# Optimization experiments

Hardware: AMD Instinct MI355X
Metric: run time of the kernel (lower is better)

## Reference

```python
import jax, jax.numpy as jnp
import numpy as np
from jax import lax

EPS = 1e-5

def conv3x3(x, w):
    # x: [B,C,H,W], w: [O,C,3,3]
    return lax.conv_general_dilated(x, w, (1, 1), ((1, 1), (1, 1)),
                                    dimension_numbers=("NCHW", "OIHW", "NCHW"))

def convbnrelu(x, w, bn):
    gamma, beta, mean, var = bn  # each [C]
    y = conv3x3(x, w)
    scale = (gamma / jnp.sqrt(var + EPS))[:, None, None]
    shift = (beta - mean * gamma / jnp.sqrt(var + EPS))[:, None, None]
    return jax.nn.relu(y * scale + shift)

def conv1x1(x, w, b):
    # w: [O,C,1,1], b: [O]
    return jnp.einsum("bchw,oc->bohw", x, w[:, :, 0, 0]) + b[:, None, None]

def pam(x, wb, bb, wc, bc, wd, bd, alpha, lfm=None):
    B, C, H, W = x.shape
    N = H * W
    q = conv1x1(x, wb, bb)
    k = conv1x1(x, wc, bc)
    v = conv1x1(x, wd, bd)
    if lfm is not None:  # VFAM: qkv flags all 1 -> multiply q, k, v
        q = q * lfm
        k = k * lfm
        v = v * lfm
    fb = q.reshape(B, -1, N).transpose(0, 2, 1)           # [B,N,Cq]
    fc = k.reshape(B, -1, N)                              # [B,Cq,N]
    attn = jax.nn.softmax(jnp.matmul(fb, fc), axis=-1)    # [B,N,N]
    fd = v.reshape(B, C, N)                               # [B,C,N]
    fe = jnp.matmul(fd, attn.transpose(0, 2, 1)).reshape(B, C, H, W)
    return alpha * fe + x

def cam(x, beta):
    B, C, H, W = x.shape
    N = H * W
    fa = x.reshape(B, C, N)
    attn = jnp.matmul(fa, fa.transpose(0, 2, 1))          # [B,C,C]
    attn = jnp.max(attn, axis=-1, keepdims=True) - attn
    attn = jax.nn.softmax(attn, axis=-1)
    fe = jnp.matmul(attn, fa).reshape(B, C, H, W)
    return beta * fe + x

def setup_inputs() -> dict:
    key = jax.random.key(0)
    ks = iter(jax.random.split(key, 64))
    B, Cin, H, W = 2, 2048, 64, 64
    Cmid = Cin // 4         # 512
    Cq = Cmid // 8          # 64
    nclass = 19

    def bn_pack(C):
        g = jnp.ones((C,)) + 0.1 * jax.random.normal(next(ks), (C,))
        b = 0.1 * jax.random.normal(next(ks), (C,))
        m = 0.1 * jax.random.normal(next(ks), (C,))
        v = jax.random.uniform(next(ks), (C,), minval=0.5, maxval=1.5)
        return jnp.stack([g, b, m, v])  # [4,C]

    def conv_w(O, I, kk):
        return jax.random.normal(next(ks), (O, I, kk, kk)) * (1.0 / np.sqrt(I * kk * kk))

    inp = {
        "x": jax.random.normal(next(ks), (B, Cin, H, W)),
        "loss_factor_map": jax.random.uniform(next(ks), (H, W)),
        "wp1": conv_w(Cmid, Cin, 3), "bnp1": bn_pack(Cmid),
        "wp2": conv_w(Cmid, Cmid, 3), "bnp2": bn_pack(Cmid),
        "wc1": conv_w(Cmid, Cin, 3), "bnc1": bn_pack(Cmid),
        "wc2": conv_w(Cmid, Cmid, 3), "bnc2": bn_pack(Cmid),
        "wv1": conv_w(Cmid, Cin, 3), "bnv1": bn_pack(Cmid),
        "wv2": conv_w(Cmid, Cmid, 3), "bnv2": bn_pack(Cmid),
        "pam_wb": conv_w(Cq, Cmid, 1), "pam_bb": jnp.zeros((Cq,)),
        "pam_wc": conv_w(Cq, Cmid, 1), "pam_bc": jnp.zeros((Cq,)),
        "pam_wd": conv_w(Cmid, Cmid, 1), "pam_bd": jnp.zeros((Cmid,)),
        "pam_alpha": 0.3 * jnp.ones((1,)),
        "cam_beta": 0.3 * jnp.ones((1,)),
        "vfam_wb": conv_w(Cq, Cmid, 1), "vfam_bb": jnp.zeros((Cq,)),
        "vfam_wc": conv_w(Cq, Cmid, 1), "vfam_bc": jnp.zeros((Cq,)),
        "vfam_wd": conv_w(Cmid, Cmid, 1), "vfam_bd": jnp.zeros((Cmid,)),
        "vfam_alpha": 0.3 * jnp.ones((1,)),
        "out_w": conv_w(nclass, Cmid, 1), "out_b": jnp.zeros((nclass,)),
        "p3_w": conv_w(nclass, Cmid, 1), "p3_b": jnp.zeros((nclass,)),
        "c3_w": conv_w(nclass, Cmid, 1), "c3_b": jnp.zeros((nclass,)),
    }
    return inp

def reference(x, loss_factor_map,
              wp1, bnp1, wp2, bnp2, wc1, bnc1, wc2, bnc2, wv1, bnv1, wv2, bnv2,
              pam_wb, pam_bb, pam_wc, pam_bc, pam_wd, pam_bd, pam_alpha,
              cam_beta,
              vfam_wb, vfam_bb, vfam_wc, vfam_bc, vfam_wd, vfam_bd, vfam_alpha,
              out_w, out_b, p3_w, p3_b, c3_w, c3_b):
    lfm = loss_factor_map[None, None, :, :]  # (1,1,H,W)
    # Position branch
    fp = convbnrelu(x, wp1, bnp1)
    fp = pam(fp, pam_wb, pam_bb, pam_wc, pam_bc, pam_wd, pam_bd, pam_alpha)
    fp = convbnrelu(fp, wp2, bnp2)
    # Channel branch
    fc = convbnrelu(x, wc1, bnc1)
    fc = cam(fc, cam_beta)
    fc = convbnrelu(fc, wc2, bnc2)
    # Visual-field branch (qkv_vfa_flag = [1,1,1])
    fv = convbnrelu(x, wv1, bnv1)
    fv = pam(fv, vfam_wb, vfam_bb, vfam_wc, vfam_bc, vfam_wd, vfam_bd, vfam_alpha, lfm=lfm)
    fv = convbnrelu(fv, wv2, bnv2)
    # Fusion + heads (Dropout in eval mode = identity)
    fusion = fp + fc + fv
    fusion_out = conv1x1(fusion, out_w, out_b)
    p_out = conv1x1(fp, p3_w, p3_b)
    c_out = conv1x1(fc, c3_w, c3_b)
    return (fusion_out, p_out, c_out)
```

## Files before the change

kernel.cpp:

```cpp
#include <hip/hip_runtime.h>

typedef unsigned short u16;
typedef short s16x8 __attribute__((ext_vector_type(8)));
typedef u16 u16x8 __attribute__((ext_vector_type(8)));
typedef u16 u16x4 __attribute__((ext_vector_type(4)));
typedef float f32x4 __attribute__((ext_vector_type(4)));

#define DEV __device__ __forceinline__

DEV float bf2f(u16 x) { unsigned v = ((unsigned)x) << 16; float f; __builtin_memcpy(&f, &v, 4); return f; }
DEV u16 f2bf(float f) { unsigned u; __builtin_memcpy(&u, &f, 4); u += 0x7FFFu + ((u >> 16) & 1u); return (u16)(u >> 16); }

DEV void gload16(const u16* g, u16* l) {
  __builtin_amdgcn_global_load_lds((const __attribute__((address_space(1))) void*)g,
                                   (__attribute__((address_space(3))) void*)l, 16, 0, 0);
}

__global__ void detect_dtype(const u16* __restrict__ x, int* __restrict__ flag) {
  int tid = threadIdx.x;
  float mx = 0.f;
  for (int i = tid; i < 4096; i += 256) mx = fmaxf(mx, fabsf(bf2f(x[i])));
  __shared__ float red[4];
  int wave = tid >> 6, lane = tid & 63;
  for (int off = 32; off; off >>= 1) mx = fmaxf(mx, __shfl_xor(mx, off));
  if (lane == 0) red[wave] = mx;
  __syncthreads();
  if (tid == 0) {
    mx = fmaxf(fmaxf(red[0], red[1]), fmaxf(red[2], red[3]));
    *flag = (mx > 1e4f) ? 1 : 0;
  }
}

struct CvBatch {
  const void* src[28];
  unsigned dstOff[28];
  unsigned n[28];
  unsigned chunkStart[29];
  int cnt;
};

__global__ __launch_bounds__(256) void convert_batch(CvBatch cb, u16* __restrict__ dstBase,
                                                     const int* __restrict__ flag) {
  const int isF = *flag;
  const unsigned bid = blockIdx.x;
  int j = 0;
  while (bid >= cb.chunkStart[j + 1]) ++j;
  const unsigned base = (bid - cb.chunkStart[j]) * 2048 + threadIdx.x * 8;
  const unsigned n = cb.n[j];
  if (base >= n) return;
  u16* dst = dstBase + cb.dstOff[j];
  const void* src = cb.src[j];
  if (base + 8 <= n) {
    u16x8 v;
    if (isF) {
      const float* f = (const float*)src;
#pragma unroll
      for (int k = 0; k < 8; ++k) v[k] = f2bf(f[base + k]);
    } else {
      v = *(const u16x8*)&((const u16*)src)[base];
    }
    *(u16x8*)&dst[base] = v;
  } else {
    for (unsigned i = base; i < n; ++i)
      dst[i] = isF ? f2bf(((const float*)src)[i]) : ((const u16*)src)[i];
  }
}

__global__ void bn_prep(const u16* __restrict__ cbn, float* __restrict__ out) {
  int w = blockIdx.x;
  const u16* bn = cbn + w * 2048;
  int c = threadIdx.x;
  float g = bf2f(bn[c]), be = bf2f(bn[512 + c]), m = bf2f(bn[1024 + c]), v = bf2f(bn[1536 + c]);
  float sc = g * rsqrtf(v + 1e-5f);
  out[w * 1024 + c] = sc;
  out[w * 1024 + 512 + c] = be - m * sc;
}

struct Repack3P { const void* src[3]; u16* dst[3]; };

__global__ __launch_bounds__(256) void repack_w3(Repack3P rp, int I, int Ishift,
                                                 const int* __restrict__ flag) {
  const int isF = *flag;
  const void* w = rp.src[blockIdx.z];
  u16* wr = rp.dst[blockIdx.z];
  size_t idx = ((size_t)blockIdx.x * 256 + threadIdx.x) * 8;
  int i0 = (int)(idx & (size_t)(I - 1));
  int t = (int)(idx >> Ishift);
  int o = t / 9, kk = t - o * 9;
  u16x8 v;
  if (isF) {
    const float* f = (const float*)w;
#pragma unroll
    for (int j = 0; j < 8; ++j) v[j] = f2bf(f[((size_t)o * I + i0 + j) * 9 + kk]);
  } else {
    const u16* bsrc = (const u16*)w;
#pragma unroll
    for (int j = 0; j < 8; ++j) v[j] = bsrc[((size_t)o * I + i0 + j) * 9 + kk];
  }
  *(u16x8*)&wr[idx] = v;
}

__global__ __launch_bounds__(256) void zero_border(u16* __restrict__ base, int CIN) {
  int p = blockIdx.x, b = blockIdx.y;
  int py, px;
  if (p < 66)       { py = 0;        px = p; }
  else if (p < 132) { py = 65;       px = p - 66; }
  else if (p < 196) { py = p - 131;  px = 0; }
  else              { py = p - 195;  px = 65; }
  u16* d = base + (((size_t)b * 66 + py) * 66 + px) * (size_t)CIN;
  for (int i = threadIdx.x * 8; i < CIN; i += 2048) {
    u16x8 z;
#pragma unroll
    for (int k = 0; k < 8; ++k) z[k] = 0;
    *(u16x8*)&d[i] = z;
  }
}

__global__ __launch_bounds__(256) void pad_nchw(const void* __restrict__ x, u16* __restrict__ xpad,
                                                const int* __restrict__ flag) {
  __shared__ u16 t[64][72];
  const int isF = *flag;
  int c0 = blockIdx.x * 64, h = blockIdx.y, b = blockIdx.z;
  int tid = threadIdx.x;
#pragma unroll
  for (int i = 0; i < 2; ++i) {
    int idx = i * 256 + tid;
    int cc = idx >> 3, ww = (idx & 7) * 8;
    size_t base = (((size_t)(b * 2048 + c0 + cc) * 64) + h) * 64 + ww;
    u16x8 v;
    if (isF) {
      const float* fx = (const float*)x;
#pragma unroll
      for (int j = 0; j < 8; ++j) v[j] = f2bf(fx[base + j]);
    } else {
      v = *(const u16x8*)&((const u16*)x)[base];
    }
    *(u16x8*)&t[cc][ww] = v;
  }
  __syncthreads();
#pragma unroll
  for (int i = 0; i < 2; ++i) {
    int idx = i * 256 + tid;
    int ww = idx >> 3, cc = (idx & 7) * 8;
    u16x8 v;
#pragma unroll
    for (int j = 0; j < 8; ++j) v[j] = t[cc + j][ww];
    *(u16x8*)&xpad[(((size_t)b * 66 + h + 1) * 66 + ww + 1) * 2048 + c0 + cc] = v;
  }
}

__global__ __launch_bounds__(256) void transpose64(const u16* __restrict__ src, u16* __restrict__ dst,
                                                   int R, int C) {
  __shared__ u16 t[64][72];
  int r0 = blockIdx.x * 64, c0 = blockIdx.y * 64;
  const u16* s = src + (size_t)blockIdx.z * R * C;
  u16* d = dst + (size_t)blockIdx.z * R * C;
  int tid = threadIdx.x;
#pragma unroll
  for (int i = 0; i < 2; ++i) {
    int idx = i * 256 + tid;
    int rr = idx >> 3, cc = (idx & 7) * 8;
    u16x8 v = *(const u16x8*)&s[(size_t)(r0 + rr) * C + c0 + cc];
    *(u16x8*)&t[rr][cc] = v;
  }
  __syncthreads();
#pragma unroll
  for (int i = 0; i < 2; ++i) {
    int idx = i * 256 + tid;
    int cc = idx >> 3, rr = (idx & 7) * 8;
    u16x8 v;
#pragma unroll
    for (int j = 0; j < 8; ++j) v[j] = t[rr + j][cc];
    *(u16x8*)&d[(size_t)(c0 + cc) * R + r0 + rr] = v;
  }
}

struct GemmP {
  const u16* A; const u16* B;
  long aBatch, bBatch;
  int M, N, K;
  u16* out; long outBatch; int ldOut;
  const u16* bias;
  const u16* rowscale;
  const u16* residual; long resBatch; int ldRes;
  const u16* alphaPtr;
  float* outF; long outFBatch;
  const u16* B2; const u16* bias2; u16* out2;
};

template <int BM, int BN, int EPI>
__global__ __launch_bounds__(256) void gemm_nt(GemmP p) {
  static_assert(EPI != 2 || BM >= BN, "EPI2 LDS bounce needs BM>=BN");
  constexpr int AH = BM * 32, BH = BN * 32;
  __shared__ __align__(16) u16 lsBuf[(BM + BN) * 64];
  u16* lA = lsBuf;
  u16* lB = lsBuf + BM * 64;
  const int tid = threadIdx.x;
  int bz = blockIdx.z;
  const u16* Bsel = p.B;
  const u16* biasSel = p.bias;
  u16* outSel = p.out;
  if (EPI == 0 && p.out2) {
    const int h = gridDim.z >> 1;
    if (bz >= h) { bz -= h; Bsel = p.B2; biasSel = p.bias2; outSel = p.out2; }
  }
  const int m0 = blockIdx.x * BM, n0 = blockIdx.y * BN;
  const u16* A = p.A + (size_t)bz * p.aBatch;
  const u16* Bp = Bsel + (size_t)bz * p.bBatch;
  const int wave = tid >> 6, lane = tid & 63;
  const int quad = lane >> 4, r16 = lane & 15;
  const int wm = (wave >> 1) * (BM / 2), wn = (wave & 1) * (BN / 2);
  constexpr int TM = BM / 32, TN = BN / 32;
  f32x4 acc[TM][TN] = {};
  const int srow = tid >> 2, sch = (tid & 3) * 8;
  const int K = p.K;
  for (int k0 = 0; k0 < K; k0 += 64) {
    __syncthreads();
#pragma unroll
    for (int i = 0; i < BM / 64; ++i) {
      const size_t ga = (size_t)(m0 + i * 64 + srow) * K + k0 + sch;
      gload16(&A[ga], lA + i * 2048 + wave * 512);
      gload16(&A[ga + 32], lA + AH + i * 2048 + wave * 512);
    }
#pragma unroll
    for (int i = 0; i < BN / 64; ++i) {
      const size_t gb = (size_t)(n0 + i * 64 + srow) * K + k0 + sch;
      gload16(&Bp[gb], lB + i * 2048 + wave * 512);
      gload16(&Bp[gb + 32], lB + BH + i * 2048 + wave * 512);
    }
    __syncthreads();
#pragma unroll
    for (int q = 0; q < 2; ++q) {
      s16x8 av[TM], bv[TN];
#pragma unroll
      for (int t = 0; t < TM; ++t)
        av[t] = *(const s16x8*)&lA[q * AH + (wm + t * 16 + r16) * 32 + quad * 8];
#pragma unroll
      for (int t = 0; t < TN; ++t)
        bv[t] = *(const s16x8*)&lB[q * BH + (wn + t * 16 + r16) * 32 + quad * 8];
#pragma unroll
      for (int i = 0; i < TM; ++i)
#pragma unroll
        for (int j = 0; j < TN; ++j)
          acc[i][j] = __builtin_amdgcn_mfma_f32_16x16x32_bf16(av[i], bv[j], acc[i][j], 0, 0, 0);
    }
  }
  if constexpr (EPI == 2) {
    float* lsF = (float*)lsBuf;
#pragma unroll
    for (int i = 0; i < TM; ++i) {
      __syncthreads();
#pragma unroll
      for (int j = 0; j < TN; ++j) {
        const int col = wn + j * 16 + r16;
#pragma unroll
        for (int r = 0; r < 4; ++r) {
          const int rowL = (wave >> 1) * 16 + quad * 4 + r;
          lsF[rowL * BN + col] = acc[i][j][r];
        }
      }
      __syncthreads();
      constexpr int PASSES = (32 * BN) / 1024;
#pragma unroll
      for (int pp = 0; pp < PASSES; ++pp) {
        const int lin = (pp * 256 + tid) * 4;
        const int rowL = lin / BN, col = lin & (BN - 1);
        const int gm = m0 + (rowL >> 4) * (BM / 2) + i * 16 + (rowL & 15);
        *(f32x4*)&p.outF[(size_t)bz * p.outFBatch + (size_t)gm * p.ldOut + (n0 + col)] =
            *(const f32x4*)&lsF[lin];
      }
    }
    return;
  }
  float alpha = 0.f;
  if (EPI == 3) alpha = bf2f(p.alphaPtr[0]);
#pragma unroll
  for (int i = 0; i < TM; ++i) {
#pragma unroll
    for (int j = 0; j < TN; ++j) {
      const int nn = n0 + wn + j * 16 + r16;
      float bia = 0.f;
      if ((EPI == 0 || EPI == 1) && biasSel) bia = bf2f(biasSel[nn]);
#pragma unroll
      for (int r = 0; r < 4; ++r) {
        const int mm = m0 + wm + i * 16 + quad * 4 + r;
        float v = acc[i][j][r];
        if (EPI == 0) {
          v += bia;
          if (p.rowscale) v *= bf2f(p.rowscale[mm]);
          outSel[(size_t)bz * p.outBatch + (size_t)mm * p.ldOut + nn] = f2bf(v);
        } else if (EPI == 1) {
          v += bia;
          if (p.rowscale) v *= bf2f(p.rowscale[mm]);
          p.out[(size_t)bz * p.outBatch + (size_t)nn * p.ldOut + mm] = f2bf(v);
        } else {
          float res = bf2f(p.residual[(size_t)bz * p.resBatch + (size_t)mm * p.ldRes + nn]);
          v = alpha * v + res;
          const int py = mm >> 6, px = mm & 63;
          p.out[(size_t)bz * p.outBatch + ((size_t)(py + 1) * 66 + (px + 1)) * p.ldOut + nn] = f2bf(v);
        }
      }
    }
  }
}

struct Conv3P {
  const u16* in[3];
  const u16* wr[3];
  u16* out[3];
  const float* bn;
};

template <int CIN>
__global__ __launch_bounds__(256) void conv3x3_k(Conv3P p) {
  __shared__ u16 lA[8192], lB[8192];
  const int tid = threadIdx.x;
  const int z = blockIdx.z, ci = z >> 1, b = z & 1;
  const int m0 = blockIdx.x * 128, n0 = blockIdx.y * 128;
  const u16* __restrict__ xin = p.in[ci];
  const u16* __restrict__ wr = p.wr[ci];
  const int wave = tid >> 6, lane = tid & 63;
  const int quad = lane >> 4, r16 = lane & 15;
  const int wm = (wave >> 1) * 64, wn = (wave & 1) * 64;
  f32x4 acc[4][4] = {};
  const int srow = tid >> 2, sch = (tid & 3) * 8;
  const int p0 = m0 + srow, p1 = p0 + 64;
  const size_t a0 = (((size_t)b * 66 + (p0 >> 6)) * 66 + (p0 & 63)) * CIN + sch;
  const size_t a1 = (((size_t)b * 66 + (p1 >> 6)) * 66 + (p1 & 63)) * CIN + sch;
  const size_t b0 = ((size_t)(n0 + srow) * 9) * CIN + sch;
  const size_t b1 = ((size_t)(n0 + 64 + srow) * 9) * CIN + sch;
  u16* la0 = &lA[wave * 512];
  u16* la1 = &lA[2048 + wave * 512];
  u16* la2 = &lA[4096 + wave * 512];
  u16* la3 = &lA[6144 + wave * 512];
  u16* lb0 = &lB[wave * 512];
  u16* lb1 = &lB[2048 + wave * 512];
  u16* lb2 = &lB[4096 + wave * 512];
  u16* lb3 = &lB[6144 + wave * 512];
  for (int c = 0; c < CIN; c += 64) {
    for (int kh = 0; kh < 3; ++kh) {
      for (int kw = 0; kw < 3; ++kw) {
        const size_t soff = ((size_t)kh * 66 + kw) * CIN + c;
        const size_t woff = (size_t)(kh * 3 + kw) * CIN + c;
        __syncthreads();
        gload16(&xin[a0 + soff], la0);
        gload16(&xin[a1 + soff], la1);
        gload16(&xin[a0 + soff + 32], la2);
        gload16(&xin[a1 + soff + 32], la3);
        gload16(&wr[b0 + woff], lb0);
        gload16(&wr[b1 + woff], lb1);
        gload16(&wr[b0 + woff + 32], lb2);
        gload16(&wr[b1 + woff + 32], lb3);
        __syncthreads();
#pragma unroll
        for (int q = 0; q < 2; ++q) {
          s16x8 av[4], bv[4];
#pragma unroll
          for (int t = 0; t < 4; ++t)
            av[t] = *(const s16x8*)&lA[q * 4096 + (wm + t * 16 + r16) * 32 + quad * 8];
#pragma unroll
          for (int t = 0; t < 4; ++t)
            bv[t] = *(const s16x8*)&lB[q * 4096 + (wn + t * 16 + r16) * 32 + quad * 8];
#pragma unroll
          for (int i = 0; i < 4; ++i)
#pragma unroll
            for (int j = 0; j < 4; ++j)
              acc[i][j] = __builtin_amdgcn_mfma_f32_16x16x32_bf16(av[i], bv[j], acc[i][j], 0, 0, 0);
        }
      }
    }
  }
  u16* __restrict__ out = p.out[ci];
  const float* bnS = p.bn + ci * 1024;
#pragma unroll
  for (int i = 0; i < 4; ++i) {
#pragma unroll
    for (int j = 0; j < 4; ++j) {
      const int nn = n0 + wn + j * 16 + r16;
      const float s = bnS[nn], sh = bnS[512 + nn];
#pragma unroll
      for (int r = 0; r < 4; ++r) {
        const int mm = m0 + wm + i * 16 + quad * 4 + r;
        float v = fmaxf(acc[i][j][r] * s + sh, 0.f);
        out[((size_t)b * 4096 + mm) * 512 + nn] = f2bf(v);
      }
    }
  }
}

__global__ __launch_bounds__(256) void softmax4096(const float* __restrict__ S, u16* __restrict__ P) {
  int row = blockIdx.x, tid = threadIdx.x;
  const float* sr = S + (size_t)row * 4096;
  f32x4 v[4];
  float mx = -3.4e38f;
#pragma unroll
  for (int i = 0; i < 4; ++i) {
    v[i] = *(const f32x4*)&sr[(i * 256 + tid) * 4];
    mx = fmaxf(mx, fmaxf(fmaxf(v[i][0], v[i][1]), fmaxf(v[i][2], v[i][3])));
  }
  __shared__ float red[8];
  int wave = tid >> 6, lane = tid & 63;
  for (int off = 32; off; off >>= 1) mx = fmaxf(mx, __shfl_xor(mx, off));
  if (lane == 0) red[wave] = mx;
  __syncthreads();
  mx = fmaxf(fmaxf(red[0], red[1]), fmaxf(red[2], red[3]));
  float sum = 0.f;
#pragma unroll
  for (int i = 0; i < 4; ++i)
#pragma unroll
    for (int j = 0; j < 4; ++j) { float e = __expf(v[i][j] - mx); v[i][j] = e; sum += e; }
  for (int off = 32; off; off >>= 1) sum += __shfl_xor(sum, off);
  if (lane == 0) red[4 + wave] = sum;
  __syncthreads();
  sum = red[4] + red[5] + red[6] + red[7];
  float inv = 1.f / sum;
  u16* pr = P + (size_t)row * 4096;
#pragma unroll
  for (int i = 0; i < 4; ++i) {
    u16x4 ov;
#pragma unroll
    for (int j = 0; j < 4; ++j) ov[j] = f2bf(v[i][j] * inv);
    *(u16x4*)&pr[(i * 256 + tid) * 4] = ov;
  }
}

__global__ __launch_bounds__(256) void softmax_cam(const float* __restrict__ S, u16* __restrict__ P) {
  int row = blockIdx.x, tid = threadIdx.x;
  const float* sr = S + (size_t)row * 512;
  float a = sr[tid], b = sr[tid + 256];
  __shared__ float red[12];
  int wave = tid >> 6, lane = tid & 63;
  float mx = fmaxf(a, b);
  for (int off = 32; off; off >>= 1) mx = fmaxf(mx, __shfl_xor(mx, off));
  if (lane == 0) red[wave] = mx;
  __syncthreads();
  float M1 = fmaxf(fmaxf(red[0], red[1]), fmaxf(red[2], red[3]));
  float mn = fminf(a, b);
  for (int off = 32; off; off >>= 1) mn = fminf(mn, __shfl_xor(mn, off));
  if (lane == 0) red[4 + wave] = mn;
  __syncthreads();
  float m2 = M1 - fminf(fminf(red[4], red[5]), fminf(red[6], red[7]));
  float e0 = __expf((M1 - a) - m2), e1 = __expf((M1 - b) - m2);
  float sum = e0 + e1;
  for (int off = 32; off; off >>= 1) sum += __shfl_xor(sum, off);
  if (lane == 0) red[8 + wave] = sum;
  __syncthreads();
  sum = red[8] + red[9] + red[10] + red[11];
  float inv = 1.f / sum;
  P[(size_t)row * 512 + tid] = f2bf(e0 * inv);
  P[(size_t)row * 512 + tid + 256] = f2bf(e1 * inv);
}

__global__ __launch_bounds__(256) void final_out_k(const u16* __restrict__ fp2, const u16* __restrict__ fc2,
                                                   const u16* __restrict__ fv2,
                                                   const u16* ow, const u16* ob, const u16* pw,
                                                   const u16* pb, const u16* cw, const u16* cb,
                                                   void* __restrict__ out, const int* __restrict__ flag) {
  __shared__ float wl[19 * 512];
  int tid = threadIdx.x, which = blockIdx.y;
  const u16* W = which == 0 ? ow : which == 1 ? pw : cw;
  const u16* Bb = which == 0 ? ob : which == 1 ? pb : cb;
  for (int i = tid; i < 19 * 512; i += 256) wl[i] = bf2f(W[i]);
  __syncthreads();
  int pix = blockIdx.x * 256 + threadIdx.x;
  size_t rb = (size_t)pix * 512;
  float acc[19];
#pragma unroll
  for (int o = 0; o < 19; ++o) acc[o] = 0.f;
  for (int c = 0; c < 512; c += 8) {
    float xs[8];
    if (which == 0) {
      u16x8 a = *(const u16x8*)&fp2[rb + c];
      u16x8 d = *(const u16x8*)&fc2[rb + c];
      u16x8 e = *(const u16x8*)&fv2[rb + c];
#pragma unroll
      for (int j = 0; j < 8; ++j) xs[j] = bf2f(a[j]) + bf2f(d[j]) + bf2f(e[j]);
    } else {
      const u16* src = which == 1 ? fp2 : fc2;
      u16x8 a = *(const u16x8*)&src[rb + c];
#pragma unroll
      for (int j = 0; j < 8; ++j) xs[j] = bf2f(a[j]);
    }
#pragma unroll
    for (int o = 0; o < 19; ++o) {
      const float* wv = &wl[o * 512 + c];
#pragma unroll
      for (int j = 0; j < 8; ++j) acc[o] += xs[j] * wv[j];
    }
  }
  int b = pix >> 12, n = pix & 4095;
  const int isF32 = *flag;
#pragma unroll
  for (int o = 0; o < 19; ++o) {
    size_t idx = (size_t)which * 155648 + ((size_t)(b * 19 + o)) * 4096 + n;
    float v = acc[o] + bf2f(Bb[o]);
    if (isF32) ((float*)out)[idx] = v;
    else ((u16*)out)[idx] = f2bf(v);
  }
}

static const size_t OFF_XPAD  = 0;
static const size_t OFF_WR1A  = 35684352;
static const size_t OFF_WR1B  = 54558720;
static const size_t OFF_WR1C  = 73433088;
static const size_t OFF_ARENA = 92307456;
static const size_t OFF_S     = 0;
static const size_t OFF_P     = 67108864;
static const size_t OFF_FP1   = 125861888;
static const size_t OFF_FC1   = 134250496;
static const size_t OFF_FV1   = 142639104;
static const size_t OFF_FC1T  = 151027712;
static const size_t OFF_QT    = 159416320;
static const size_t OFF_KT    = 160464896;
static const size_t OFF_VT    = 161513472;
static const size_t OFF_WRSA  = 151027712;
static const size_t OFF_WRSB  = 155746304;
static const size_t OFF_WRSC  = 161513472;
static const size_t OFF_PADP  = 169902080;
static const size_t OFF_PADC  = 178823168;
static const size_t OFF_PADV  = 187744256;
static const size_t OFF_FP2   = 125861888;
static const size_t OFF_FC2   = 134250496;
static const size_t OFF_FV2   = 142639104;
static const size_t OFF_SC    = 196665344;
static const size_t OFF_PC    = 198762496;
static const size_t OFF_BN    = 199811072;
static const size_t OFF_FLAG  = 199835648;
static const size_t OFF_SMALL = 199835904;
static const size_t SO_CBN    = 0;
static const size_t SO_PWB    = 12288;
static const size_t SO_PBB    = 45056;
static const size_t SO_PWC    = 45120;
static const size_t SO_PBC    = 77888;
static const size_t SO_PWD    = 77952;
static const size_t SO_PBD    = 340096;
static const size_t SO_PAL    = 340608;
static const size_t SO_CBETA  = 340624;
static const size_t SO_VWB    = 340640;
static const size_t SO_VBB    = 373408;
static const size_t SO_VWC    = 373472;
static const size_t SO_VBC    = 406240;
static const size_t SO_VWD    = 406304;
static const size_t SO_VBD    = 668448;
static const size_t SO_VAL    = 668960;
static const size_t SO_OW     = 668976;
static const size_t SO_OB     = 678704;
static const size_t SO_PW3    = 678736;
static const size_t SO_PB3    = 688464;
static const size_t SO_CW3    = 688496;
static const size_t SO_CB3    = 698224;
static const size_t SO_LFM    = 698256;
static const size_t SO_END    = 702352;
static const size_t WS_NEEDED = OFF_SMALL + SO_END * 2;

extern "C" void kernel_launch(void* const* d_in, const int* in_sizes, int n_in,
                              void* d_out, int out_size, void* d_ws, size_t ws_size,
                              hipStream_t stream) {
  if (ws_size < WS_NEEDED) return;
  (void)in_sizes; (void)n_in; (void)out_size;

  char* ws = (char*)d_ws;
  u16* xpad   = (u16*)(ws + OFF_XPAD);
  u16* wr1a   = (u16*)(ws + OFF_WR1A);
  u16* wr1b   = (u16*)(ws + OFF_WR1B);
  u16* wr1c   = (u16*)(ws + OFF_WR1C);
  float* S    = (float*)(ws + OFF_S);
  u16* P      = (u16*)(ws + OFF_P);
  u16* fp1    = (u16*)(ws + OFF_FP1);
  u16* fc1    = (u16*)(ws + OFF_FC1);
  u16* fv1    = (u16*)(ws + OFF_FV1);
  u16* fc1T   = (u16*)(ws + OFF_FC1T);
  u16* qt     = (u16*)(ws + OFF_QT);
  u16* kt     = (u16*)(ws + OFF_KT);
  u16* vT     = (u16*)(ws + OFF_VT);
  u16* wrsa   = (u16*)(ws + OFF_WRSA);
  u16* wrsb   = (u16*)(ws + OFF_WRSB);
  u16* wrsc   = (u16*)(ws + OFF_WRSC);
  u16* padP   = (u16*)(ws + OFF_PADP);
  u16* padC   = (u16*)(ws + OFF_PADC);
  u16* padV   = (u16*)(ws + OFF_PADV);
  u16* fp2    = (u16*)(ws + OFF_FP2);
  u16* fc2    = (u16*)(ws + OFF_FC2);
  u16* fv2    = (u16*)(ws + OFF_FV2);
  float* Sc   = (float*)(ws + OFF_SC);
  u16* Pc     = (u16*)(ws + OFF_PC);
  float* bnb  = (float*)(ws + OFF_BN);
  int* flag   = (int*)(ws + OFF_FLAG);
  u16* sm     = (u16*)(ws + OFF_SMALL);

  detect_dtype<<<1, 256, 0, stream>>>((const u16*)d_in[0], flag);
  {
    CvBatch cb{};
    int jn = 0; unsigned chunks = 0;
    auto addJob = [&](int i, size_t dstOff, unsigned n) {
      cb.src[jn] = d_in[i]; cb.dstOff[jn] = (unsigned)dstOff; cb.n[jn] = n;
      cb.chunkStart[jn] = chunks; chunks += (n + 2047) / 2048; ++jn;
    };
    addJob(3,  SO_CBN + 0 * 2048, 2048);
    addJob(7,  SO_CBN + 1 * 2048, 2048);
    addJob(11, SO_CBN + 2 * 2048, 2048);
    addJob(5,  SO_CBN + 3 * 2048, 2048);
    addJob(9,  SO_CBN + 4 * 2048, 2048);
    addJob(13, SO_CBN + 5 * 2048, 2048);
    addJob(14, SO_PWB, 32768);  addJob(15, SO_PBB, 64);
    addJob(16, SO_PWC, 32768);  addJob(17, SO_PBC, 64);
    addJob(18, SO_PWD, 262144); addJob(19, SO_PBD, 512);
    addJob(20, SO_PAL, 1);      addJob(21, SO_CBETA, 1);
    addJob(22, SO_VWB, 32768);  addJob(23, SO_VBB, 64);
    addJob(24, SO_VWC, 32768);  addJob(25, SO_VBC, 64);
    addJob(26, SO_VWD, 262144); addJob(27, SO_VBD, 512);
    addJob(28, SO_VAL, 1);
    addJob(29, SO_OW, 9728);    addJob(30, SO_OB, 19);
    addJob(31, SO_PW3, 9728);   addJob(32, SO_PB3, 19);
    addJob(33, SO_CW3, 9728);   addJob(34, SO_CB3, 19);
    addJob(1,  SO_LFM, 4096);
    cb.cnt = jn; cb.chunkStart[jn] = chunks;
    convert_batch<<<chunks, 256, 0, stream>>>(cb, sm, flag);
  }

  bn_prep<<<6, 512, 0, stream>>>(sm + SO_CBN, bnb);

  zero_border<<<dim3(260, 2), 256, 0, stream>>>(xpad, 2048);
  pad_nchw<<<dim3(32, 64, 2), 256, 0, stream>>>(d_in[0], xpad, flag);

  {
    Repack3P rp{};
    rp.src[0] = d_in[2];  rp.dst[0] = wr1a;
    rp.src[1] = d_in[6];  rp.dst[1] = wr1b;
    rp.src[2] = d_in[10]; rp.dst[2] = wr1c;
    repack_w3<<<dim3(4608, 1, 3), 256, 0, stream>>>(rp, 2048, 11, flag);
  }
  {
    Conv3P c{};
    c.in[0] = xpad; c.in[1] = xpad; c.in[2] = xpad;
    c.wr[0] = wr1a; c.wr[1] = wr1b; c.wr[2] = wr1c;
    c.out[0] = fp1; c.out[1] = fc1; c.out[2] = fv1;
    c.bn = bnb;
    conv3x3_k<2048><<<dim3(32, 4, 6), 256, 0, stream>>>(c);
  }

  auto runPam = [&](const u16* src, const u16* wb, const u16* bb, const u16* wck, const u16* bck,
                    const u16* wd, const u16* bd, const u16* alphaP, const u16* rs, u16* padOut) {
    GemmP g{};
    g.A = src; g.aBatch = 2097152; g.B = wb; g.bBatch = 0; g.M = 4096; g.N = 64; g.K = 512;
    g.out = qt; g.outBatch = 262144; g.ldOut = 64; g.bias = bb; g.rowscale = rs;
    g.B2 = wck; g.bias2 = bck; g.out2 = kt;
    gemm_nt<64, 64, 0><<<dim3(64, 1, 4), 256, 0, stream>>>(g);
    GemmP gv{};
    gv.A = src; gv.aBatch = 2097152; gv.B = wd; gv.bBatch = 0; gv.M = 4096; gv.N = 512; gv.K = 512;
    gv.out = vT; gv.outBatch = 2097152; gv.ldOut = 4096; gv.bias = bd; gv.rowscale = rs;
    gemm_nt<64, 128, 1><<<dim3(64, 4, 2), 256, 0, stream>>>(gv);
    zero_border<<<dim3(260, 2), 256, 0, stream>>>(padOut, 512);
    for (int b = 0; b < 2; ++b) {
      GemmP gs{};
      gs.A = qt + (size_t)b * 262144; gs.B = kt + (size_t)b * 262144;
      gs.M = 4096; gs.N = 4096; gs.K = 64;
      gs.outF = S; gs.outFBatch = 0; gs.ldOut = 4096;
      gemm_nt<128, 128, 2><<<dim3(32, 32, 1), 256, 0, stream>>>(gs);
      softmax4096<<<4096, 256, 0, stream>>>(S, P);
      GemmP gf{};
      gf.A = P; gf.aBatch = 0; gf.B = vT + (size_t)b * 2097152; gf.bBatch = 0;
      gf.M = 4096; gf.N = 512; gf.K = 4096;
      gf.out = padOut + (size_t)b * 2230272; gf.outBatch = 0; gf.ldOut = 512;
      gf.residual = src + (size_t)b * 2097152; gf.resBatch = 0; gf.ldRes = 512;
      gf.alphaPtr = alphaP;
      gemm_nt<128, 64, 3><<<dim3(32, 8, 1), 256, 0, stream>>>(gf);
    }
  };
  runPam(fp1, sm + SO_PWB, sm + SO_PBB, sm + SO_PWC, sm + SO_PBC, sm + SO_PWD, sm + SO_PBD,
         sm + SO_PAL, nullptr, padP);
  runPam(fv1, sm + SO_VWB, sm + SO_VBB, sm + SO_VWC, sm + SO_VBC, sm + SO_VWD, sm + SO_VBD,
         sm + SO_VAL, sm + SO_LFM, padV);

  transpose64<<<dim3(64, 8, 2), 256, 0, stream>>>(fc1, fc1T, 4096, 512);
  {
    GemmP g{};
    g.A = fc1T; g.aBatch = 2097152; g.B = fc1T; g.bBatch = 2097152;
    g.M = 512; g.N = 512; g.K = 4096;
    g.outF = Sc; g.outFBatch = 262144; g.ldOut = 512;
    gemm_nt<64, 64, 2><<<dim3(8, 8, 2), 256, 0, stream>>>(g);
  }
  softmax_cam<<<1024, 256, 0, stream>>>(Sc, Pc);
  zero_border<<<dim3(260, 2), 256, 0, stream>>>(padC, 512);
  {
    GemmP g{};
    g.A = fc1; g.aBatch = 2097152; g.B = Pc; g.bBatch = 262144;
    g.M = 4096; g.N = 512; g.K = 512;
    g.out = padC; g.outBatch = 2230272; g.ldOut = 512;
    g.residual = fc1; g.resBatch = 2097152; g.ldRes = 512;
    g.alphaPtr = sm + SO_CBETA;
    gemm_nt<128, 128, 3><<<dim3(32, 4, 2), 256, 0, stream>>>(g);
  }

  {
    Repack3P rp{};
    rp.src[0] = d_in[4];  rp.dst[0] = wrsa;
    rp.src[1] = d_in[8];  rp.dst[1] = wrsb;
    rp.src[2] = d_in[12]; rp.dst[2] = wrsc;
    repack_w3<<<dim3(1152, 1, 3), 256, 0, stream>>>(rp, 512, 9, flag);
  }
  {
    Conv3P c{};
    c.in[0] = padP; c.in[1] = padC; c.in[2] = padV;
    c.wr[0] = wrsa; c.wr[1] = wrsb; c.wr[2] = wrsc;
    c.out[0] = fp2; c.out[1] = fc2; c.out[2] = fv2;
    c.bn = bnb + 3 * 1024;
    conv3x3_k<512><<<dim3(32, 4, 6), 256, 0, stream>>>(c);
  }

  final_out_k<<<dim3(32, 3), 256, 0, stream>>>(fp2, fc2, fv2, sm + SO_OW, sm + SO_OB,
                                               sm + SO_PW3, sm + SO_PB3, sm + SO_CW3, sm + SO_CB3,
                                               d_out, flag);
}
```

Measured before the change: 1.497 ms.

## Double-buffer LDS tiles in gemm_nt with K-step 32 prefetch

Replaces the single-buffered 64-wide K loop with a two-buffer LDS pipeline that issues the next 32-wide K slice's global-to-LDS loads before computing on the current one. One barrier per step replaces the two barriers around load and compute, aiming to hide global load latency behind MFMA work. The trade-off is a halved K step, so there are twice as many iterations and barriers, and the loads are still only fenced by the same barrier, so the overlap may be limited.

Measured after the change: 1.482 ms. Within noise of the previous version (-1.0%).

```diff
diff --git a/kernel.cpp b/kernel.cpp
--- a/kernel.cpp
+++ b/kernel.cpp
@@ -191,10 +191,8 @@
 template <int BM, int BN, int EPI>
 __global__ __launch_bounds__(256) void gemm_nt(GemmP p) {
   static_assert(EPI != 2 || BM >= BN, "EPI2 LDS bounce needs BM>=BN");
-  constexpr int AH = BM * 32, BH = BN * 32;
-  __shared__ __align__(16) u16 lsBuf[(BM + BN) * 64];
-  u16* lA = lsBuf;
-  u16* lB = lsBuf + BM * 64;
+  constexpr int HB = (BM + BN) * 32;
+  __shared__ __align__(16) u16 ls[2][HB];
   const int tid = threadIdx.x;
   int bz = blockIdx.z;
   const u16* Bsel = p.B;
@@ -214,39 +212,37 @@
   f32x4 acc[TM][TN] = {};
   const int srow = tid >> 2, sch = (tid & 3) * 8;
   const int K = p.K;
-  for (int k0 = 0; k0 < K; k0 += 64) {
+  auto stage = [&](int buf, int k0) {
+#pragma unroll
+    for (int i = 0; i < BM / 64; ++i)
+      gload16(&A[(size_t)(m0 + i * 64 + srow) * K + k0 + sch], &ls[buf][i * 2048 + wave * 512]);
+#pragma unroll
+    for (int i = 0; i < BN / 64; ++i)
+      gload16(&Bp[(size_t)(n0 + i * 64 + srow) * K + k0 + sch],
+              &ls[buf][BM * 32 + i * 2048 + wave * 512]);
+  };
+  stage(0, 0);
+  __syncthreads();
+  int cur = 0;
+  for (int k0 = 0; k0 < K; k0 += 32) {
+    if (k0 + 32 < K) stage(cur ^ 1, k0 + 32);
+    const u16* lA = &ls[cur][0];
+    const u16* lB = &ls[cur][BM * 32];
+    s16x8 av[TM], bv[TN];
+#pragma unroll
+    for (int t = 0; t < TM; ++t) av[t] = *(const s16x8*)&lA[(wm + t * 16 + r16) * 32 + quad * 8];
+#pragma unroll
+    for (int t = 0; t < TN; ++t) bv[t] = *(const s16x8*)&lB[(wn + t * 16 + r16) * 32 + quad * 8];
+#pragma unroll
+    for (int i = 0; i < TM; ++i)
+#pragma unroll
+      for (int j = 0; j < TN; ++j)
+        acc[i][j] = __builtin_amdgcn_mfma_f32_16x16x32_bf16(av[i], bv[j], acc[i][j], 0, 0, 0);
     __syncthreads();
-#pragma unroll
-    for (int i = 0; i < BM / 64; ++i) {
-      const size_t ga = (size_t)(m0 + i * 64 + srow) * K + k0 + sch;
-      gload16(&A[ga], lA + i * 2048 + wave * 512);
-      gload16(&A[ga + 32], lA + AH + i * 2048 + wave * 512);
-    }
-#pragma unroll
-    for (int i = 0; i < BN / 64; ++i) {
-      const size_t gb = (size_t)(n0 + i * 64 + srow) * K + k0 + sch;
-      gload16(&Bp[gb], lB + i * 2048 + wave * 512);
-      gload16(&Bp[gb + 32], lB + BH + i * 2048 + wave * 512);
-    }
-    __syncthreads();
-#pragma unroll
-    for (int q = 0; q < 2; ++q) {
-      s16x8 av[TM], bv[TN];
-#pragma unroll
-      for (int t = 0; t < TM; ++t)
-        av[t] = *(const s16x8*)&lA[q * AH + (wm + t * 16 + r16) * 32 + quad * 8];
-#pragma unroll
-      for (int t = 0; t < TN; ++t)
-        bv[t] = *(const s16x8*)&lB[q * BH + (wn + t * 16 + r16) * 32 + quad * 8];
-#pragma unroll
-      for (int i = 0; i < TM; ++i)
-#pragma unroll
-        for (int j = 0; j < TN; ++j)
-          acc[i][j] = __builtin_amdgcn_mfma_f32_16x16x32_bf16(av[i], bv[j], acc[i][j], 0, 0, 0);
-    }
+    cur ^= 1;
   }
   if constexpr (EPI == 2) {
-    float* lsF = (float*)lsBuf;
+    float* lsF = (float*)&ls[0][0];
 #pragma unroll
     for (int i = 0; i < TM; ++i) {
       __syncthreads();
```
